# Kernel optimization log

Hardware: AMD Instinct MI355X
Metric: run time of the kernel (lower is better)

## Reference

```python
import jax, jax.numpy as jnp
import numpy as np

DIM, HEADS, WS = 192, 8, 8
B, H, W = 4, 256, 256


def conv2d(x, w, b=None, padding=((0, 0), (0, 0)), groups=1):
    y = jax.lax.conv_general_dilated(
        x, w, window_strides=(1, 1), padding=padding,
        dimension_numbers=("NCHW", "OIHW", "NCHW"), feature_group_count=groups)
    if b is not None:
        y = y + b[None, :, None, None]
    return y


def setup_inputs() -> dict:
    key = jax.random.key(0)
    ks = jax.random.split(key, 16)
    d = DIM
    s = 0.02
    return {
        "x": jax.random.normal(ks[0], (B, d, H, W), jnp.float32),
        "w_dww": jax.random.normal(ks[1], (d, 1, 1, 11), jnp.float32) * s,
        "b_dww": jnp.zeros((d,), jnp.float32),
        "w_dwh": jax.random.normal(ks[2], (d, 1, 11, 1), jnp.float32) * s,
        "b_dwh": jnp.zeros((d,), jnp.float32),
        "w_dwhw": jax.random.normal(ks[3], (2 * d, 1, 3, 3), jnp.float32) * s,
        "b_dwhw": jnp.zeros((2 * d,), jnp.float32),
        "w_conv1": jax.random.normal(ks[4], (d, 2 * d, 1, 1), jnp.float32) * s,
        "w_qkv": jax.random.normal(ks[5], (3 * d, d, 1, 1), jnp.float32) * s,
        "w_qkvdw": jax.random.normal(ks[6], (3 * d, 1, 3, 3), jnp.float32) * s,
        "w_conv2": jax.random.normal(ks[7], (d, d, 1, 1), jnp.float32) * s,
        "w_conv3": jax.random.normal(ks[8], (d, d, 1, 1), jnp.float32) * s,
        "w_conv4a": jax.random.normal(ks[9], (d, d, 1, 1), jnp.float32) * s,
        "w_conv4b": jax.random.normal(ks[10], (d, 1, 3, 3), jnp.float32) * s,
        "w_proj": jax.random.normal(ks[11], (d, 2 * d, 1, 1), jnp.float32) * s,
        "temperature": jnp.ones((HEADS, 1, 1), jnp.float32),
    }


def reference(x, w_dww, b_dww, w_dwh, b_dwh, w_dwhw, b_dwhw, w_conv1,
              w_qkv, w_qkvdw, w_conv2, w_conv3, w_conv4a, w_conv4b,
              w_proj, temperature):
    b, c, h, w = x.shape
    d, heads, ws = DIM, HEADS, WS

    # high-frequency branch: strip depthwise convs -> 3x3 depthwise -> 1x1
    hw_cat = jnp.concatenate([
        conv2d(x, w_dww, b_dww, padding=((0, 0), (5, 5)), groups=d),
        conv2d(x, w_dwh, b_dwh, padding=((5, 5), (0, 0)), groups=d)], axis=1)
    high = conv2d(hw_cat, w_dwhw, b_dwhw, padding=((1, 1), (1, 1)), groups=2 * d)
    high = conv2d(high, w_conv1)  # [b, d, h, w]

    # low-frequency branch: avg-pool downsample then channel attention
    x_down = x.reshape(b, c, h // ws, ws, w // ws, ws).mean(axis=(3, 5))
    qkv = conv2d(x_down, w_qkv)
    qkv = conv2d(qkv, w_qkvdw, padding=((1, 1), (1, 1)), groups=3 * d)
    q, k, v = jnp.split(qkv, 3, axis=1)

    hd, wd = h // ws, w // ws
    ch = d // heads
    q = q.reshape(b, heads, ch, hd * wd)
    k = k.reshape(b, heads, ch, hd * wd)
    q = q / jnp.maximum(jnp.linalg.norm(q, axis=-1, keepdims=True), 1e-12)
    k = k / jnp.maximum(jnp.linalg.norm(k, axis=-1, keepdims=True), 1e-12)
    attn = jnp.einsum("bhcn,bhdn->bhcd", q, k) * temperature[None]  # [b,heads,ch,ch]
    attn = jax.nn.softmax(attn, axis=-1)

    # pooling gate on v (global 1x1) then modulate full-res conv4(x)
    v_max = jnp.max(v, axis=(2, 3), keepdims=True)
    v_avg = jnp.mean(v, axis=(2, 3), keepdims=True)
    v_gate = conv2d(v_max, w_conv2) + conv2d(v_avg, w_conv3)  # [b, d, 1, 1]
    x4 = conv2d(conv2d(x, w_conv4a), w_conv4b, padding=((1, 1), (1, 1)), groups=d)
    v_full = v_gate * x4  # [b, d, h, w]

    v_full = v_full.reshape(b, heads, ch, h * w)
    low = jnp.einsum("bhcd,bhdn->bhcn", attn, v_full).reshape(b, d, h, w)

    return conv2d(jnp.concatenate([high, low], axis=1), w_proj)
```

## Files before the change

### kernel.cpp

```cpp
#include <hip/hip_runtime.h>
#include <hip/hip_bf16.h>

typedef __hip_bfloat16 bf16;
typedef __attribute__((ext_vector_type(8))) short s8v;
typedef __attribute__((ext_vector_type(4))) float f4;

#define DEVI __device__ __forceinline__

DEVI f4 mfma16(s8v a, s8v b, f4 c){
  return __builtin_amdgcn_mfma_f32_16x16x32_bf16(a, b, c, 0, 0, 0);
}

constexpr int NPIX = 65536;
constexpr int NDOWN = 1024;

__global__ void k_cast_w(const float* __restrict__ w1, const float* __restrict__ w4a,
                         const float* __restrict__ wp, const float* __restrict__ wq,
                         bf16* __restrict__ out){
  int i = blockIdx.x*256 + threadIdx.x;
  if (i < 73728) out[i] = __float2bfloat16(w1[i]);
  else if (i < 110592) out[i] = __float2bfloat16(w4a[i - 73728]);
  else if (i < 184320) out[i] = __float2bfloat16(wp[i - 110592]);
  else if (i < 294912) out[i] = __float2bfloat16(wq[i - 184320]);
}

__global__ void k_pack_x(const float* __restrict__ x, bf16* __restrict__ xp){
  __shared__ float t[8][1032];
  int b = blockIdx.z, cb = blockIdx.y, ns = blockIdx.x, tid = threadIdx.x;
  const float* src = x + ((size_t)(b*192 + cb*8))*NPIX + ns*1024;
  #pragma unroll
  for (int i = 0; i < 8; ++i){
    float4 v = *(const float4*)(src + (size_t)i*NPIX + tid*4);
    *(float4*)&t[i][tid*4] = v;
  }
  __syncthreads();
  bf16* dst = xp + (((size_t)(b*24 + cb))*NPIX + ns*1024)*8;
  #pragma unroll
  for (int j = 0; j < 4; ++j){
    int p = j*256 + tid;
    alignas(16) bf16 c8[8];
    #pragma unroll
    for (int i = 0; i < 8; ++i) c8[i] = __float2bfloat16(t[i][p]);
    *(uint4*)(dst + (size_t)p*8) = *(const uint4*)c8;
  }
}

__global__ void k_pool(const bf16* __restrict__ xp, bf16* __restrict__ xdp){
  __shared__ float red[8][32][8];
  int b = blockIdx.z, cb = blockIdx.y, hd = blockIdx.x, tid = threadIdx.x;
  int r = tid >> 5, wd = tid & 31;
  const bf16* src = xp + (((size_t)(b*24 + cb))*NPIX + (hd*8 + r)*256 + wd*8)*8;
  float acc[8] = {0,0,0,0,0,0,0,0};
  #pragma unroll
  for (int ww = 0; ww < 8; ++ww){
    uint4 raw = *(const uint4*)(src + ww*8);
    const bf16* c8 = (const bf16*)&raw;
    #pragma unroll
    for (int i = 0; i < 8; ++i) acc[i] += __bfloat162float(c8[i]);
  }
  #pragma unroll
  for (int i = 0; i < 8; ++i) red[r][wd][i] = acc[i];
  __syncthreads();
  if (tid < 32){
    alignas(16) bf16 o8[8];
    #pragma unroll
    for (int i = 0; i < 8; ++i){
      float s = 0.f;
      #pragma unroll
      for (int rr = 0; rr < 8; ++rr) s += red[rr][tid][i];
      o8[i] = __float2bfloat16(s * (1.0f/64.0f));
    }
    *(uint4*)(xdp + (((size_t)(b*24 + cb))*NDOWN + hd*32 + tid)*8) = *(const uint4*)o8;
  }
}

template<int K, bool PLANAR>
__launch_bounds__(256, 2)
__global__ void k_gemm(const bf16* __restrict__ Bp, const bf16* __restrict__ W,
                       void* __restrict__ outp, int npix, int outkb){
  constexpr int KB8 = K/8;
  constexpr int NIT = K/64;
  __shared__ bf16 As[96*72];
  __shared__ bf16 Bs[128*72];
  int tid = threadIdx.x;
  int b = blockIdx.z;
  int m0 = blockIdx.y*96;
  int n0 = blockIdx.x*128;
  int wave = tid >> 6, lane = tid & 63;
  int wm = wave >> 1, wn = wave & 1;
  int lr = lane & 15, kg = lane >> 4;
  f4 acc[3][4] = {};
  const size_t bK = (size_t)b * KB8;
  for (int kt = 0; kt < NIT; ++kt){
    {
      int idx = tid;
      #pragma unroll
      for (int j = 0; j < 3; ++j, idx += 256){
        int m = idx >> 3, kc = idx & 7;
        *(uint4*)&As[m*72 + kc*8] = *(const uint4*)(W + (size_t)(m0 + m)*K + kt*64 + kc*8);
      }
      idx = tid;
      #pragma unroll
      for (int j = 0; j < 4; ++j, idx += 256){
        int kb = idx >> 7, n = idx & 127;
        *(uint4*)&Bs[n*72 + kb*8] = *(const uint4*)(Bp + ((bK + kt*8 + kb)*npix + n0 + n)*8);
      }
    }
    __syncthreads();
    #pragma unroll
    for (int kk = 0; kk < 2; ++kk){
      s8v af[3]; s8v bfr[4];
      int ko = kk*32 + kg*8;
      #pragma unroll
      for (int mf = 0; mf < 3; ++mf) af[mf] = *(const s8v*)&As[(wm*48 + mf*16 + lr)*72 + ko];
      #pragma unroll
      for (int nf = 0; nf < 4; ++nf) bfr[nf] = *(const s8v*)&Bs[(wn*64 + nf*16 + lr)*72 + ko];
      #pragma unroll
      for (int mf = 0; mf < 3; ++mf)
        #pragma unroll
        for (int nf = 0; nf < 4; ++nf)
          acc[mf][nf] = mfma16(af[mf], bfr[nf], acc[mf][nf]);
    }
    __syncthreads();
  }
  int quad = lane >> 4;
  #pragma unroll
  for (int mf = 0; mf < 3; ++mf){
    int mb = m0 + wm*48 + mf*16 + quad*4;
    #pragma unroll
    for (int nf = 0; nf < 4; ++nf){
      int n = n0 + wn*64 + nf*16 + lr;
      if constexpr (PLANAR){
        float* o = (float*)outp;
        #pragma unroll
        for (int r2 = 0; r2 < 4; ++r2)
          o[((size_t)(b*outkb + mb + r2))*npix + n] = acc[mf][nf][r2];
      } else {
        bf16* o = (bf16*)outp;
        alignas(8) bf16 v4[4];
        #pragma unroll
        for (int r2 = 0; r2 < 4; ++r2) v4[r2] = __float2bfloat16(acc[mf][nf][r2]);
        *(uint2*)(o + ((size_t)(b*outkb + (mb >> 3))*npix + n)*8 + (mb & 7)) = *(const uint2*)v4;
      }
    }
  }
}

__global__ void k_high_dw(const bf16* __restrict__ xp,
    const float* __restrict__ wdww, const float* __restrict__ bdww,
    const float* __restrict__ wdwh, const float* __restrict__ bdwh,
    const float* __restrict__ w3, const float* __restrict__ b3,
    bf16* __restrict__ hw3p){
  __shared__ bf16 xs[28*28*8];
  __shared__ float dwwt[18*18*8];
  __shared__ float dwht[18*18*8];
  int t = blockIdx.x, cb = blockIdx.y, b = blockIdx.z, tid = threadIdx.x;
  int r0 = (t >> 4)*16, c0 = (t & 15)*16;
  const bf16* src = xp + ((size_t)(b*24 + cb))*NPIX*8;
  for (int i = tid; i < 784; i += 256){
    int r = i/28, c = i - r*28;
    int gr = r0 + r - 6, gc = c0 + c - 6;
    uint4 v = {0,0,0,0};
    if ((unsigned)gr < 256u && (unsigned)gc < 256u)
      v = *(const uint4*)(src + ((size_t)(gr*256 + gc))*8);
    *(uint4*)&xs[i*8] = v;
  }
  __syncthreads();
  {
    int ch = tid & 7, pr = tid >> 3;
    int cg = cb*8 + ch;
    float ww[11], wh[11];
    #pragma unroll
    for (int j = 0; j < 11; ++j){ ww[j] = wdww[cg*11 + j]; wh[j] = wdwh[cg*11 + j]; }
    float bw = bdww[cg], bh = bdwh[cg];
    for (int p = pr; p < 324; p += 32){
      int r = p/18, c = p - r*18;
      int gr = r0 + r - 1, gc = c0 + c - 1;
      float vww = 0.f, vwh = 0.f;
      if ((unsigned)gr < 256u && (unsigned)gc < 256u){
        vww = bw; vwh = bh;
        #pragma unroll
        for (int j = 0; j < 11; ++j){
          vww += ww[j]*__bfloat162float(xs[((r+5)*28 + c + j)*8 + ch]);
          vwh += wh[j]*__bfloat162float(xs[((r+j)*28 + c + 5)*8 + ch]);
        }
      }
      dwwt[p*8 + ch] = vww;
      dwht[p*8 + ch] = vwh;
    }
  }
  __syncthreads();
  {
    int r = tid >> 4, c = tid & 15;
    int n = (r0 + r)*256 + c0 + c;
    alignas(16) bf16 o1[8], o2[8];
    #pragma unroll
    for (int ch = 0; ch < 8; ++ch){
      int cg = cb*8 + ch;
      float s1 = b3[cg], s2 = b3[192 + cg];
      #pragma unroll
      for (int dr = 0; dr < 3; ++dr)
        #pragma unroll
        for (int dc = 0; dc < 3; ++dc){
          int pi = ((r + dr)*18 + c + dc)*8 + ch;
          s1 += w3[cg*9 + dr*3 + dc]         * dwwt[pi];
          s2 += w3[(192 + cg)*9 + dr*3 + dc] * dwht[pi];
        }
      o1[ch] = __float2bfloat16(s1);
      o2[ch] = __float2bfloat16(s2);
    }
    *(uint4*)(hw3p + (((size_t)(b*48 + cb))*NPIX + n)*8)      = *(const uint4*)o1;
    *(uint4*)(hw3p + (((size_t)(b*48 + 24 + cb))*NPIX + n)*8) = *(const uint4*)o2;
  }
}

__global__ void k_qkv_dw(const bf16* __restrict__ qkv0p, const float* __restrict__ wdw,
                         float* __restrict__ qkvd, float* __restrict__ vmax, float* __restrict__ vavg){
  __shared__ bf16 xs[34*34*8];
  __shared__ float red[256*8];
  int cb = blockIdx.x, b = blockIdx.y, tid = threadIdx.x;
  for (int i = tid; i < 1156; i += 256){
    int r = i/34, c = i - r*34;
    int gr = r - 1, gc = c - 1;
    uint4 v = {0,0,0,0};
    if ((unsigned)gr < 32u && (unsigned)gc < 32u)
      v = *(const uint4*)(qkv0p + (((size_t)(b*72 + cb))*NDOWN + gr*32 + gc)*8);
    *(uint4*)&xs[i*8] = v;
  }
  __syncthreads();
  float mxv[8], smv[8];
  #pragma unroll
  for (int ch = 0; ch < 8; ++ch){ mxv[ch] = -3.4e38f; smv[ch] = 0.f; }
  for (int j = 0; j < 4; ++j){
    int p = j*256 + tid;
    int r = p >> 5, c = p & 31;
    #pragma unroll
    for (int ch = 0; ch < 8; ++ch){
      float s = 0.f;
      #pragma unroll
      for (int dr = 0; dr < 3; ++dr)
        #pragma unroll
        for (int dc = 0; dc < 3; ++dc)
          s += wdw[(cb*8 + ch)*9 + dr*3 + dc] *
               __bfloat162float(xs[((r + dr)*34 + c + dc)*8 + ch]);
      qkvd[((size_t)(b*576 + cb*8 + ch))*NDOWN + p] = s;
      mxv[ch] = fmaxf(mxv[ch], s);
      smv[ch] += s;
    }
  }
  if (cb >= 48){
    #pragma unroll
    for (int ch = 0; ch < 8; ++ch) red[tid*8 + ch] = mxv[ch];
    __syncthreads();
    for (int st = 128; st > 0; st >>= 1){
      if (tid < st)
        #pragma unroll
        for (int ch = 0; ch < 8; ++ch)
          red[tid*8 + ch] = fmaxf(red[tid*8 + ch], red[(tid + st)*8 + ch]);
      __syncthreads();
    }
    if (tid < 8) vmax[b*192 + (cb - 48)*8 + tid] = red[tid];
    __syncthreads();
    #pragma unroll
    for (int ch = 0; ch < 8; ++ch) red[tid*8 + ch] = smv[ch];
    __syncthreads();
    for (int st = 128; st > 0; st >>= 1){
      if (tid < st)
        #pragma unroll
        for (int ch = 0; ch < 8; ++ch) red[tid*8 + ch] += red[(tid + st)*8 + ch];
      __syncthreads();
    }
    if (tid < 8) vavg[b*192 + (cb - 48)*8 + tid] = red[tid] * (1.0f/1024.0f);
  }
}

__global__ void k_attn(const float* __restrict__ qkvd, const float* __restrict__ temp,
                       float* __restrict__ attn){
  __shared__ float inv[48];
  __shared__ float sm[576];
  int bh = blockIdx.x;
  int b = bh >> 3, h = bh & 7;
  const float* qb = qkvd + ((size_t)(b*576 + h*24))*NDOWN;
  const float* kb = qkvd + ((size_t)(b*576 + 192 + h*24))*NDOWN;
  int tid = threadIdx.x, wave = tid >> 6, lane = tid & 63;
  for (int v = wave; v < 48; v += 4){
    const float* p = (v < 24) ? (qb + v*NDOWN) : (kb + (v - 24)*NDOWN);
    float s = 0.f;
    for (int i = lane; i < NDOWN; i += 64){ float xv = p[i]; s += xv*xv; }
    #pragma unroll
    for (int o = 32; o > 0; o >>= 1) s += __shfl_down(s, o);
    if (lane == 0) inv[v] = 1.0f / fmaxf(sqrtf(s), 1e-12f);
  }
  __syncthreads();
  float tp = temp[h];
  for (int pr = tid; pr < 576; pr += 256){
    int c = pr/24, d = pr - c*24;
    const float4* qp = (const float4*)(qb + c*NDOWN);
    const float4* kp = (const float4*)(kb + d*NDOWN);
    float s = 0.f;
    for (int i = 0; i < 256; ++i){
      float4 a = qp[i], e = kp[i];
      s += a.x*e.x + a.y*e.y + a.z*e.z + a.w*e.w;
    }
    sm[pr] = s * inv[c] * inv[24 + d] * tp;
  }
  __syncthreads();
  if (tid < 24){
    float mx = -3.4e38f;
    for (int d = 0; d < 24; ++d) mx = fmaxf(mx, sm[tid*24 + d]);
    float sum = 0.f;
    for (int d = 0; d < 24; ++d) sum += __expf(sm[tid*24 + d] - mx);
    float isum = 1.0f / sum;
    for (int d = 0; d < 24; ++d)
      attn[((size_t)bh)*576 + tid*24 + d] = __expf(sm[tid*24 + d] - mx) * isum;
  }
}

__global__ void k_gate(const float* __restrict__ vmax, const float* __restrict__ vavg,
                       const float* __restrict__ w2, const float* __restrict__ w3,
                       float* __restrict__ gate){
  __shared__ float vm[192], va[192];
  int b = blockIdx.x, tid = threadIdx.x;
  if (tid < 192){ vm[tid] = vmax[b*192 + tid]; va[tid] = vavg[b*192 + tid]; }
  __syncthreads();
  if (tid < 192){
    float s = 0.f;
    const float* w2r = w2 + tid*192;
    const float* w3r = w3 + tid*192;
    for (int k = 0; k < 192; ++k) s += w2r[k]*vm[k] + w3r[k]*va[k];
    gate[b*192 + tid] = s;
  }
}

__global__ void k_low(const bf16* __restrict__ x4ap, const float* __restrict__ attn,
                      const float* __restrict__ gate, const float* __restrict__ w4b,
                      bf16* __restrict__ hlp){
  __shared__ bf16 xt[3*18*18*8];
  __shared__ float a2[576];
  __shared__ float wt[216];
  __shared__ float vt[24*256];
  int t = blockIdx.x, h = blockIdx.y, b = blockIdx.z, tid = threadIdx.x;
  int r0 = (t >> 4)*16, c0 = (t & 15)*16;
  int ch0 = h*24;
  for (int i = tid; i < 576; i += 256)
    a2[i] = attn[((size_t)(b*8 + h))*576 + i] * gate[b*192 + ch0 + (i % 24)];
  for (int i = tid; i < 216; i += 256) wt[i] = w4b[ch0*9 + i];
  for (int i = tid; i < 972; i += 256){
    int kb = i/324, p = i - kb*324;
    int r = p/18, c = p - r*18;
    int gr = r0 + r - 1, gc = c0 + c - 1;
    uint4 v = {0,0,0,0};
    if ((unsigned)gr < 256u && (unsigned)gc < 256u)
      v = *(const uint4*)(x4ap + (((size_t)(b*24 + h*3 + kb))*NPIX + gr*256 + gc)*8);
    *(uint4*)&xt[i*8] = v;
  }
  __syncthreads();
  {
    int r = tid >> 4, c = tid & 15;
    #pragma unroll
    for (int ch = 0; ch < 24; ++ch){
      int kb = ch >> 3, ci = ch & 7;
      float s = 0.f;
      #pragma unroll
      for (int dr = 0; dr < 3; ++dr)
        #pragma unroll
        for (int dc = 0; dc < 3; ++dc)
          s += wt[ch*9 + dr*3 + dc] *
               __bfloat162float(xt[((kb*18 + r + dr)*18 + c + dc)*8 + ci]);
      vt[ch*256 + tid] = s;
    }
  }
  __syncthreads();
  {
    float o[24];
    #pragma unroll
    for (int cc = 0; cc < 24; ++cc){
      float s = 0.f;
      #pragma unroll
      for (int d = 0; d < 24; ++d) s += a2[cc*24 + d] * vt[d*256 + tid];
      o[cc] = s;
    }
    int n = (r0 + (tid >> 4))*256 + c0 + (tid & 15);
    #pragma unroll
    for (int kb = 0; kb < 3; ++kb){
      alignas(16) bf16 c8[8];
      #pragma unroll
      for (int i = 0; i < 8; ++i) c8[i] = __float2bfloat16(o[kb*8 + i]);
      *(uint4*)(hlp + (((size_t)(b*48 + 24 + h*3 + kb))*NPIX + n)*8) = *(const uint4*)c8;
    }
  }
}

extern "C" void kernel_launch(void* const* d_in, const int* in_sizes, int n_in,
                              void* d_out, int out_size, void* d_ws, size_t ws_size,
                              hipStream_t stream){
  const float* x        = (const float*)d_in[0];
  const float* w_dww    = (const float*)d_in[1];
  const float* b_dww    = (const float*)d_in[2];
  const float* w_dwh    = (const float*)d_in[3];
  const float* b_dwh    = (const float*)d_in[4];
  const float* w_dwhw   = (const float*)d_in[5];
  const float* b_dwhw   = (const float*)d_in[6];
  const float* w_conv1  = (const float*)d_in[7];
  const float* w_qkv    = (const float*)d_in[8];
  const float* w_qkvdw  = (const float*)d_in[9];
  const float* w_conv2  = (const float*)d_in[10];
  const float* w_conv3  = (const float*)d_in[11];
  const float* w_conv4a = (const float*)d_in[12];
  const float* w_conv4b = (const float*)d_in[13];
  const float* w_proj   = (const float*)d_in[14];
  const float* temp     = (const float*)d_in[15];

  char* ws = (char*)d_ws;
  size_t off = 0;
  auto take = [&](size_t bytes)->char*{
    char* r = ws + off;
    off = (off + bytes + 255) & ~(size_t)255;
    return r;
  };
  bf16*  xp    = (bf16*) take((size_t)4*192*65536*2);
  bf16*  hw3p  = (bf16*) take((size_t)4*384*65536*2);
  bf16*  hlp   = (bf16*) take((size_t)4*384*65536*2);
  bf16*  x4ap  = (bf16*) take((size_t)4*192*65536*2);
  bf16*  xdp   = (bf16*) take((size_t)4*192*1024*2);
  bf16*  qkv0p = (bf16*) take((size_t)4*576*1024*2);
  float* qkvd  = (float*)take((size_t)4*576*1024*4);
  float* attn  = (float*)take((size_t)4*8*576*4);
  float* vmax  = (float*)take((size_t)4*192*4);
  float* vavg  = (float*)take((size_t)4*192*4);
  float* gate  = (float*)take((size_t)4*192*4);
  bf16*  wbf   = (bf16*) take((size_t)294912*2);
  if (off > ws_size) return;

  k_cast_w<<<1152, 256, 0, stream>>>(w_conv1, w_conv4a, w_proj, w_qkv, wbf);
  k_pack_x<<<dim3(64,24,4), 256, 0, stream>>>(x, xp);
  k_pool<<<dim3(32,24,4), 256, 0, stream>>>(xp, xdp);
  k_gemm<192,false><<<dim3(8,6,4), 256, 0, stream>>>(xdp, wbf + 184320, qkv0p, 1024, 72);
  k_qkv_dw<<<dim3(72,4), 256, 0, stream>>>(qkv0p, w_qkvdw, qkvd, vmax, vavg);
  k_attn<<<32, 256, 0, stream>>>(qkvd, temp, attn);
  k_gate<<<4, 192, 0, stream>>>(vmax, vavg, w_conv2, w_conv3, gate);
  k_high_dw<<<dim3(256,24,4), 256, 0, stream>>>(xp, w_dww, b_dww, w_dwh, b_dwh, w_dwhw, b_dwhw, hw3p);
  k_gemm<384,false><<<dim3(512,2,4), 256, 0, stream>>>(hw3p, wbf, hlp, 65536, 48);
  k_gemm<192,false><<<dim3(512,2,4), 256, 0, stream>>>(xp, wbf + 73728, x4ap, 65536, 24);
  k_low<<<dim3(256,8,4), 256, 0, stream>>>(x4ap, attn, gate, w_conv4b, hlp);
  k_gemm<384,true><<<dim3(512,2,4), 256, 0, stream>>>(hlp, wbf + 110592, d_out, 65536, 192);
}
```

Measured before the change: 1.050 ms.

## Use direct global-to-LDS loads in GEMM and vectorize high-freq depthwise kernel

The GEMM now loads the B tile with global_load_lds straight into a [kb][n][8] shared-memory layout, which drops the register round trip, and raises the launch-bounds occupancy hint to 3 blocks. The high-frequency depthwise kernel stages weights and biases in shared memory as channel pairs. Each thread now handles all 8 channels of a pixel, with 16-byte LDS loads, bf16 unpacking and paired FMAs, and the intermediate buffers are padded to a stride of 10. The risks are LDS bank conflicts in the new unpadded B layout, register pressure from the tighter launch bounds, and uneven work (324 pixels over 256 threads) in the strip stage.

```diff
diff --git a/kernel.cpp b/kernel.cpp
--- a/kernel.cpp
+++ b/kernel.cpp
@@ -9,6 +9,23 @@
 
 DEVI f4 mfma16(s8v a, s8v b, f4 c){
   return __builtin_amdgcn_mfma_f32_16x16x32_bf16(a, b, c, 0, 0, 0);
+}
+
+DEVI void gl_lds16(const void* g, void* l){
+  __builtin_amdgcn_global_load_lds(
+      (const __attribute__((address_space(1))) void*)g,
+      (__attribute__((address_space(3))) void*)l, 16, 0, 0);
+}
+
+DEVI float2 pkfma(float2 a, float2 b, float2 c){
+  return make_float2(fmaf(a.x, b.x, c.x), fmaf(a.y, b.y, c.y));
+}
+
+DEVI void unp8(uint4 v, float2* f){
+  f[0] = make_float2(__uint_as_float(v.x << 16), __uint_as_float(v.x & 0xffff0000u));
+  f[1] = make_float2(__uint_as_float(v.y << 16), __uint_as_float(v.y & 0xffff0000u));
+  f[2] = make_float2(__uint_as_float(v.z << 16), __uint_as_float(v.z & 0xffff0000u));
+  f[3] = make_float2(__uint_as_float(v.w << 16), __uint_as_float(v.w & 0xffff0000u));
 }
 
 constexpr int NPIX = 65536;
@@ -75,13 +92,13 @@
 }
 
 template<int K, bool PLANAR>
-__launch_bounds__(256, 2)
+__launch_bounds__(256, 3)
 __global__ void k_gemm(const bf16* __restrict__ Bp, const bf16* __restrict__ W,
                        void* __restrict__ outp, int npix, int outkb){
   constexpr int KB8 = K/8;
   constexpr int NIT = K/64;
   __shared__ bf16 As[96*72];
-  __shared__ bf16 Bs[128*72];
+  __shared__ bf16 Bs[8*128*8];
   int tid = threadIdx.x;
   int b = blockIdx.z;
   int m0 = blockIdx.y*96;
@@ -99,22 +116,24 @@
         int m = idx >> 3, kc = idx & 7;
         *(uint4*)&As[m*72 + kc*8] = *(const uint4*)(W + (size_t)(m0 + m)*K + kt*64 + kc*8);
       }
-      idx = tid;
-      #pragma unroll
-      for (int j = 0; j < 4; ++j, idx += 256){
-        int kb = idx >> 7, n = idx & 127;
-        *(uint4*)&Bs[n*72 + kb*8] = *(const uint4*)(Bp + ((bK + kt*8 + kb)*npix + n0 + n)*8);
-      }
+    }
+    #pragma unroll
+    for (int tsk = 0; tsk < 4; ++tsk){
+      int t = wave + tsk*4;
+      int kb = t >> 1, nh = (t & 1)*64;
+      const bf16* g = Bp + ((bK + kt*8 + kb)*npix + n0 + nh + lane)*8;
+      gl_lds16(g, &Bs[((size_t)kb*128 + nh)*8]);
     }
     __syncthreads();
     #pragma unroll
     for (int kk = 0; kk < 2; ++kk){
       s8v af[3]; s8v bfr[4];
       int ko = kk*32 + kg*8;
+      int kbb = kk*4 + kg;
       #pragma unroll
       for (int mf = 0; mf < 3; ++mf) af[mf] = *(const s8v*)&As[(wm*48 + mf*16 + lr)*72 + ko];
       #pragma unroll
-      for (int nf = 0; nf < 4; ++nf) bfr[nf] = *(const s8v*)&Bs[(wn*64 + nf*16 + lr)*72 + ko];
+      for (int nf = 0; nf < 4; ++nf) bfr[nf] = *(const s8v*)&Bs[(kbb*128 + wn*64 + nf*16 + lr)*8];
       #pragma unroll
       for (int mf = 0; mf < 3; ++mf)
         #pragma unroll
@@ -152,10 +171,31 @@
     const float* __restrict__ w3, const float* __restrict__ b3,
     bf16* __restrict__ hw3p){
   __shared__ bf16 xs[28*28*8];
-  __shared__ float dwwt[18*18*8];
-  __shared__ float dwht[18*18*8];
+  __shared__ float dwwt[324*10];
+  __shared__ float dwht[324*10];
+  __shared__ float2 wwL[11][4], whL[11][4];
+  __shared__ float2 w3L[2][9][4];
+  __shared__ float2 bwL[4], bhL[4], b3L[2][4];
   int t = blockIdx.x, cb = blockIdx.y, b = blockIdx.z, tid = threadIdx.x;
   int r0 = (t >> 4)*16, c0 = (t & 15)*16;
+  int cg0 = cb*8;
+  if (tid < 44){
+    int j = tid >> 2, q = tid & 3;
+    wwL[j][q] = make_float2(wdww[(cg0+2*q)*11 + j], wdww[(cg0+2*q+1)*11 + j]);
+    whL[j][q] = make_float2(wdwh[(cg0+2*q)*11 + j], wdwh[(cg0+2*q+1)*11 + j]);
+  } else if (tid < 116){
+    int i = tid - 44;
+    int cv = i/36, rr = i - cv*36;
+    int tap = rr >> 2, q = rr & 3;
+    int row = cv*192 + cg0;
+    w3L[cv][tap][q] = make_float2(w3[(row+2*q)*9 + tap], w3[(row+2*q+1)*9 + tap]);
+  } else if (tid < 120){
+    int q = tid - 116;
+    bwL[q] = make_float2(bdww[cg0+2*q], bdww[cg0+2*q+1]);
+    bhL[q] = make_float2(bdwh[cg0+2*q], bdwh[cg0+2*q+1]);
+    b3L[0][q] = make_float2(b3[cg0+2*q], b3[cg0+2*q+1]);
+    b3L[1][q] = make_float2(b3[192+cg0+2*q], b3[192+cg0+2*q+1]);
+  }
   const bf16* src = xp + ((size_t)(b*24 + cb))*NPIX*8;
   for (int i = tid; i < 784; i += 256){
     int r = i/28, c = i - r*28;
@@ -166,51 +206,70 @@
     *(uint4*)&xs[i*8] = v;
   }
   __syncthreads();
+  for (int p = tid; p < 324; p += 256){
+    int r = p/18, c = p - r*18;
+    int gr = r0 + r - 1, gc = c0 + c - 1;
+    float2 aw[4], ah[4];
+    if ((unsigned)gr < 256u && (unsigned)gc < 256u){
+      #pragma unroll
+      for (int q = 0; q < 4; ++q){ aw[q] = bwL[q]; ah[q] = bhL[q]; }
+      int bw_ = (r+5)*28 + c;
+      #pragma unroll
+      for (int j = 0; j < 11; ++j){
+        uint4 v = *(const uint4*)&xs[(bw_ + j)*8];
+        float2 f[4]; unp8(v, f);
+        #pragma unroll
+        for (int q = 0; q < 4; ++q) aw[q] = pkfma(f[q], wwL[j][q], aw[q]);
+      }
+      int bh_ = r*28 + c + 5;
+      #pragma unroll
+      for (int j = 0; j < 11; ++j){
+        uint4 v = *(const uint4*)&xs[(bh_ + j*28)*8];
+        float2 f[4]; unp8(v, f);
+        #pragma unroll
+        for (int q = 0; q < 4; ++q) ah[q] = pkfma(f[q], whL[j][q], ah[q]);
+      }
+    } else {
+      #pragma unroll
+      for (int q = 0; q < 4; ++q){ aw[q] = make_float2(0.f,0.f); ah[q] = make_float2(0.f,0.f); }
+    }
+    #pragma unroll
+    for (int q = 0; q < 4; ++q){
+      *(float2*)&dwwt[p*10 + 2*q] = aw[q];
+      *(float2*)&dwht[p*10 + 2*q] = ah[q];
+    }
+  }
+  __syncthreads();
   {
-    int ch = tid & 7, pr = tid >> 3;
-    int cg = cb*8 + ch;
-    float ww[11], wh[11];
-    #pragma unroll
-    for (int j = 0; j < 11; ++j){ ww[j] = wdww[cg*11 + j]; wh[j] = wdwh[cg*11 + j]; }
-    float bw = bdww[cg], bh = bdwh[cg];
-    for (int p = pr; p < 324; p += 32){
-      int r = p/18, c = p - r*18;
-      int gr = r0 + r - 1, gc = c0 + c - 1;
-      float vww = 0.f, vwh = 0.f;
-      if ((unsigned)gr < 256u && (unsigned)gc < 256u){
-        vww = bw; vwh = bh;
-        #pragma unroll
-        for (int j = 0; j < 11; ++j){
-          vww += ww[j]*__bfloat162float(xs[((r+5)*28 + c + j)*8 + ch]);
-          vwh += wh[j]*__bfloat162float(xs[((r+j)*28 + c + 5)*8 + ch]);
+    int r = tid >> 4, c = tid & 15;
+    float2 o1[4], o2[4];
+    #pragma unroll
+    for (int q = 0; q < 4; ++q){ o1[q] = b3L[0][q]; o2[q] = b3L[1][q]; }
+    #pragma unroll
+    for (int dr = 0; dr < 3; ++dr)
+      #pragma unroll
+      for (int dc = 0; dc < 3; ++dc){
+        int pp = ((r+dr)*18 + c+dc)*10;
+        int tap = dr*3 + dc;
+        #pragma unroll
+        for (int q = 0; q < 4; ++q){
+          float2 v1 = *(const float2*)&dwwt[pp + 2*q];
+          float2 v2 = *(const float2*)&dwht[pp + 2*q];
+          o1[q] = pkfma(v1, w3L[0][tap][q], o1[q]);
+          o2[q] = pkfma(v2, w3L[1][tap][q], o2[q]);
         }
       }
-      dwwt[p*8 + ch] = vww;
-      dwht[p*8 + ch] = vwh;
-    }
-  }
-  __syncthreads();
-  {
-    int r = tid >> 4, c = tid & 15;
     int n = (r0 + r)*256 + c0 + c;
-    alignas(16) bf16 o1[8], o2[8];
-    #pragma unroll
-    for (int ch = 0; ch < 8; ++ch){
-      int cg = cb*8 + ch;
-      float s1 = b3[cg], s2 = b3[192 + cg];
-      #pragma unroll
-      for (int dr = 0; dr < 3; ++dr)
-        #pragma unroll
-        for (int dc = 0; dc < 3; ++dc){
-          int pi = ((r + dr)*18 + c + dc)*8 + ch;
-          s1 += w3[cg*9 + dr*3 + dc]         * dwwt[pi];
-          s2 += w3[(192 + cg)*9 + dr*3 + dc] * dwht[pi];
-        }
-      o1[ch] = __float2bfloat16(s1);
-      o2[ch] = __float2bfloat16(s2);
-    }
-    *(uint4*)(hw3p + (((size_t)(b*48 + cb))*NPIX + n)*8)      = *(const uint4*)o1;
-    *(uint4*)(hw3p + (((size_t)(b*48 + 24 + cb))*NPIX + n)*8) = *(const uint4*)o2;
+    alignas(16) bf16 o1b[8], o2b[8];
+    #pragma unroll
+    for (int q = 0; q < 4; ++q){
+      o1b[2*q]   = __float2bfloat16(o1[q].x);
+      o1b[2*q+1] = __float2bfloat16(o1[q].y);
+      o2b[2*q]   = __float2bfloat16(o2[q].x);
+      o2b[2*q+1] = __float2bfloat16(o2[q].y);
+    }
+    *(uint4*)(hw3p + (((size_t)(b*48 + cb))*NPIX + n)*8)      = *(const uint4*)o1b;
+    *(uint4*)(hw3p + (((size_t)(b*48 + 24 + cb))*NPIX + n)*8) = *(const uint4*)o2b;
   }
 }
 
```

Result: slower. 2.711 ms (+158.2%).
